# Kernel optimization log

Hardware: AMD Instinct MI355X
Metric: run time of the kernel (lower is better)

The kernel has to match this reference:

```python
import jax, jax.numpy as jnp
import numpy as np

B, L, D = 4, 4096, 1024  # batch, seq, d_model == in_features == out_features
E, R = 8, 8              # n_experts, r_base
DH = D // 2              # router hidden


def setup_inputs() -> dict:
    key = jax.random.key(0)
    ks = jax.random.split(key, 8)
    s = 0.02
    return {
        "x": jax.random.normal(ks[0], (B, L, D), dtype=jnp.float32),
        "W_base": jax.random.normal(ks[1], (D, D), dtype=jnp.float32) * s,
        "router_W1": jax.random.normal(ks[2], (DH, D), dtype=jnp.float32) * s,
        "router_b1": jnp.zeros((DH,), dtype=jnp.float32),
        "router_W2": jax.random.normal(ks[3], (E, DH), dtype=jnp.float32) * s,
        "router_b2": jnp.zeros((E,), dtype=jnp.float32),
        "temperature": jnp.asarray(1.0, dtype=jnp.float32),
        "lora_A": jax.random.normal(ks[4], (E, R, D), dtype=jnp.float32) * s,
        "lora_B": jax.random.normal(ks[5], (E, D, R), dtype=jnp.float32) * s,
    }


def reference(x, W_base, router_W1, router_b1, router_W2, router_b2,
              temperature, lora_A, lora_B):
    # Base frozen linear (bias=False): [B,L,D]
    base = jnp.einsum("bld,od->blo", x, W_base)
    # Router (eval mode: dropout inactive). hidden_states = x (Identity projection).
    h = jax.nn.relu(jnp.einsum("bld,hd->blh", x, router_W1) + router_b1)
    logits = (jnp.einsum("blh,eh->ble", h, router_W2) + router_b2) / temperature
    gates = jax.nn.softmax(logits, axis=-1)  # softmax over experts, [B,L,E]
    # All experts' low-rank projections batched: x @ A_e.T -> [B,L,E,R]
    xa = jnp.einsum("bld,erd->bler", x, lora_A)
    # Gate-weighted up-projection and sum over experts: [B,L,D]
    lora_out = jnp.einsum("bler,ble,edr->bld", xa, gates, lora_B)
    return base + lora_out
```

## Files before the change

kernel.cpp:

```cpp
#include <hip/hip_runtime.h>
#include <hip/hip_bf16.h>
#include <stdint.h>
#include <math.h>


#define M_TOK 16384

typedef unsigned short u16;
typedef short bf16x8 __attribute__((ext_vector_type(8)));
typedef float f32x4 __attribute__((ext_vector_type(4)));
typedef __attribute__((address_space(3))) uint32_t lds_u32_t;
typedef __attribute__((address_space(1))) const uint32_t glb_u32_t;

__device__ __forceinline__ u16 f2bf(float f) {
  uint32_t u = __builtin_bit_cast(uint32_t, f);
  return (u16)((u + 0x7fffu + ((u >> 16) & 1u)) >> 16);
}
__device__ __forceinline__ int cvtpk(float lo, float hi) {
  int r;
  asm("v_cvt_pk_bf16_f32 %0, %1, %2" : "=v"(r) : "v"(lo), "v"(hi));
  return r;
}

#define VMCNT(n) asm volatile("s_waitcnt vmcnt(%0)" ::"i"(n) : "memory")
#define LGKM0 asm volatile("s_waitcnt lgkmcnt(0)" ::: "memory")
#define BAR asm volatile("s_barrier" ::: "memory")
#define MEMFENCE asm volatile("" ::: "memory")
#define SP(x) __builtin_amdgcn_s_setprio(x)

__global__ __launch_bounds__(256) void prep_k(const float* __restrict__ Wb,
                                              const float* __restrict__ rW1,
                                              const float* __restrict__ rW2,
                                              const float* __restrict__ loraA,
                                              const float* __restrict__ loraB,
                                              u16* __restrict__ Btb,
                                              u16* __restrict__ W1b,
                                              u16* __restrict__ W2b,
                                              u16* __restrict__ A2b) {
  const int g = blockIdx.x;
  const int tid = threadIdx.x;
  if (g < 1024) {
    int i = g * 256 + tid;
    int idx = i * 4;
    int row = idx >> 10, col = idx & 1023;
    float4 v = ((const float4*)Wb)[i];
    ushort4 o;
    o.x = f2bf(v.x); o.y = f2bf(v.y); o.z = f2bf(v.z); o.w = f2bf(v.w);
    *(ushort4*)(Btb + (size_t)row * 1088 + col) = o;
  } else if (g < 1536) {
    int i = (g - 1024) * 256 + tid;
    float4 v = ((const float4*)rW1)[i];
    ushort4 o;
    o.x = f2bf(v.x); o.y = f2bf(v.y); o.z = f2bf(v.z); o.w = f2bf(v.w);
    ((ushort4*)W1b)[i] = o;
  } else if (g < 1792) {
    int idx = (g - 1536) * 256 + tid;
    int n = idx >> 6, q = idx & 63;
    int e = q >> 3, r = q & 7;
    Btb[(size_t)n * 1088 + 1024 + q] = f2bf(loraB[((size_t)(e * 1024 + n)) * 8 + r]);
  } else if (g < 1856) {
    int i = (g - 1792) * 256 + tid;
    float4 v = ((const float4*)loraA)[i];
    ushort4 o;
    o.x = f2bf(v.x); o.y = f2bf(v.y); o.z = f2bf(v.z); o.w = f2bf(v.w);
    ((ushort4*)A2b)[i] = o;
  } else {
    int i = (g - 1856) * 256 + tid;
    int idx = i * 4;
    int row = idx >> 9, col = idx & 511;
    ushort4 o = {0, 0, 0, 0};
    if (row < 8) {
      float4 v = *(const float4*)(rW2 + (size_t)row * 512 + col);
      o.x = f2bf(v.x); o.y = f2bf(v.y); o.z = f2bf(v.z); o.w = f2bf(v.w);
    }
    ((ushort4*)W2b)[i] = o;
  }
}

__global__ __launch_bounds__(512, 2) void gemm_h(const float* __restrict__ x,
                                                 const u16* __restrict__ W1b,
                                                 const u16* __restrict__ W2bv,
                                                 u16* __restrict__ xb,
                                                 float* __restrict__ gates,
                                                 const float* __restrict__ b1,
                                                 const float* __restrict__ b2,
                                                 const float* __restrict__ temp,
                                                 const int K) {
  constexpr int ABUF = 64 * 128;
  constexpr int BBUF = 512 * 128;
  constexpr int BUFB = ABUF + BBUF;
  __shared__ __align__(16) uint8_t lds[2 * BUFB];

  const int tid = threadIdx.x;
  const int lane = tid & 63, w = tid >> 6;
  const int l15 = lane & 15, lhi = lane >> 4;
  const int xorv = (lane & 7) << 4;
  const int c0 = (lhi * 16) ^ xorv;
  const int c1 = (64 + lhi * 16) ^ xorv;

  const int f = blockIdx.x;
  const int m0 = ((f & 7) * 32 + (f >> 3)) * 64;

  const int nk = K >> 6;
  const int rot = (f >> 3) & (nk - 1);
  auto PH = [&](int l) { int lc = l < nk ? l : nk - 1; return (lc + rot) & (nk - 1); };

  const int xrow = tid >> 3, xsub = tid & 7;

  f32x4 acc[4][4] = {};
  bf16x8 af[4][2], bfv[4][2];
  float4 xA0, xA1, xB0, xB1;

  auto stageBH = [&](int ktp, int b) {
    uint8_t* dst = lds + b * BUFB + ABUF + w * 1024;
#pragma unroll
    for (int i = 0; i < 8; ++i) {
      const int off = i * 8192 + tid * 16;
      const int row = off >> 7;
      const int ss = ((off >> 4) & 7) ^ (row & 7);
      const uint8_t* g =
          (const uint8_t*)W1b + (size_t)row * 2048 + ktp * 128 + ss * 16;
      __builtin_amdgcn_global_load_lds((glb_u32_t*)g, (lds_u32_t*)(dst + i * 8192),
                                       16, 0, 0);
    }
  };
  auto issueX = [&](int ktp, float4& ra, float4& rb) {
    const float* gp = x + (size_t)(m0 + xrow) * 1024 + ktp * 64 + xsub * 8;
    ra = *(const float4*)gp;
    rb = *(const float4*)(gp + 4);
  };
  auto writeA = [&](int ktp, int b, const float4& ra, const float4& rb) {
    int4 sv;
    sv.x = cvtpk(ra.x, ra.y); sv.y = cvtpk(ra.z, ra.w);
    sv.z = cvtpk(rb.x, rb.y); sv.w = cvtpk(rb.z, rb.w);
    *(int4*)(lds + b * BUFB + xrow * 128 + ((xsub ^ (xrow & 7)) << 4)) = sv;
    *(int4*)(xb + (size_t)(m0 + xrow) * 1024 + ktp * 64 + xsub * 8) = sv;
  };
  auto loadAH = [&](const uint8_t* bufA) {
#pragma unroll
    for (int mf = 0; mf < 4; ++mf) {
      const uint8_t* pr = bufA + (mf * 16 + l15) * 128;
      af[mf][0] = *(const bf16x8*)(pr + c0);
      af[mf][1] = *(const bf16x8*)(pr + c1);
    }
  };
  auto loadBH = [&](const uint8_t* bufB) {
#pragma unroll
    for (int nf = 0; nf < 4; ++nf) {
      const uint8_t* pr = bufB + (w * 64 + nf * 16 + l15) * 128;
      bfv[nf][0] = *(const bf16x8*)(pr + c0);
      bfv[nf][1] = *(const bf16x8*)(pr + c1);
    }
  };

#define HMM()                                                                  \
  _Pragma("unroll") for (int mf = 0; mf < 4; ++mf)                             \
  _Pragma("unroll") for (int nf = 0; nf < 4; ++nf)                             \
  _Pragma("unroll") for (int ks = 0; ks < 2; ++ks)                             \
      acc[mf][nf] = __builtin_amdgcn_mfma_f32_16x16x32_bf16(                   \
          af[mf][ks], bfv[nf][ks], acc[mf][nf], 0, 0, 0);

  {
    const float* gp = x + (size_t)(m0 + xrow) * 1024 + rot * 64 + xsub * 8;
    float4 a = *(const float4*)gp, b = *(const float4*)(gp + 4);
    int4 sv;
    sv.x = cvtpk(a.x, a.y); sv.y = cvtpk(a.z, a.w);
    sv.z = cvtpk(b.x, b.y); sv.w = cvtpk(b.z, b.w);
    *(int4*)(lds + xrow * 128 + ((xsub ^ (xrow & 7)) << 4)) = sv;
    *(int4*)(xb + (size_t)(m0 + xrow) * 1024 + rot * 64 + xsub * 8) = sv;
  }
  stageBH(rot, 0);
  MEMFENCE;
  issueX(PH(1), xA0, xA1);
  VMCNT(2);
  LGKM0;
  BAR;

  const int nit = nk >> 1;
#pragma unroll 1
  for (int it = 0; it < nit; ++it) {
    const int t = it * 2;
    loadAH(lds);
    loadBH(lds + ABUF);
    stageBH(PH(t + 1), 1);
    MEMFENCE;
    issueX(PH(t + 2), xB0, xB1);
    MEMFENCE;
    VMCNT(10);
    writeA(PH(t + 1), 1, xA0, xA1);
    SP(1); HMM(); SP(0);
    LGKM0; VMCNT(3); BAR;
    loadAH(lds + BUFB);
    loadBH(lds + BUFB + ABUF);
    stageBH(PH(t + 2), 0);
    MEMFENCE;
    issueX(PH(t + 3), xA0, xA1);
    MEMFENCE;
    VMCNT(10);
    writeA(PH(t + 2), 0, xB0, xB1);
    SP(1); HMM(); SP(0);
    LGKM0; VMCNT(3); BAR;
  }

  u16* hs = (u16*)lds;
  __syncthreads();
#pragma unroll
  for (int mf = 0; mf < 4; ++mf) {
#pragma unroll
    for (int nf = 0; nf < 4; ++nf) {
      const int col = w * 64 + nf * 16 + l15;
#pragma unroll
      for (int j = 0; j < 4; ++j) {
        const int row = mf * 16 + lhi * 4 + j;
        float v = fmaxf(acc[mf][nf][j] + b1[col], 0.f);
        hs[row * 520 + col] = f2bf(v);
      }
    }
  }
  __syncthreads();
  if (w < 4) {
    f32x4 acc2 = {};
#pragma unroll
    for (int ks = 0; ks < 16; ++ks) {
      bf16x8 bfrag = *(const bf16x8*)(W2bv + (size_t)l15 * 512 + ks * 32 + lhi * 8);
      bf16x8 afrag = *(const bf16x8*)(hs + (w * 16 + l15) * 520 + ks * 32 + lhi * 8);
      acc2 = __builtin_amdgcn_mfma_f32_16x16x32_bf16(afrag, bfrag, acc2, 0, 0, 0);
    }
    if (l15 < 8) {
      float t = temp[0];
      float lg[4];
#pragma unroll
      for (int j = 0; j < 4; ++j) lg[j] = (acc2[j] + b2[l15]) / t;
      float mx[4], sm[4];
#pragma unroll
      for (int j = 0; j < 4; ++j) mx[j] = lg[j];
#pragma unroll
      for (int m = 1; m <= 4; m <<= 1)
#pragma unroll
        for (int j = 0; j < 4; ++j) mx[j] = fmaxf(mx[j], __shfl_xor(mx[j], m));
#pragma unroll
      for (int j = 0; j < 4; ++j) { lg[j] = expf(lg[j] - mx[j]); sm[j] = lg[j]; }
#pragma unroll
      for (int m = 1; m <= 4; m <<= 1)
#pragma unroll
        for (int j = 0; j < 4; ++j) sm[j] += __shfl_xor(sm[j], m);
#pragma unroll
      for (int j = 0; j < 4; ++j)
        gates[(size_t)(m0 + w * 16 + lhi * 4 + j) * 8 + l15] = lg[j] / sm[j];
    }
  }
}

__global__ __launch_bounds__(256) void gemm_w(const u16* __restrict__ A,
                                              const u16* __restrict__ Bt,
                                              const float* __restrict__ gates,
                                              u16* __restrict__ Cv) {
  constexpr int BM = 64, BN = 64, FM = 2, FN = 2, AI = 2, BI = 2;
  __shared__ u16 lds[(BM + BN) * 64];
  __shared__ float g_lds[64][8];
  u16* As = lds;
  u16* Bs = lds + BM * 64;

  const int tid = threadIdx.x;
  const int w = tid >> 6, lane = tid & 63;
  const int wr = w >> 1, wc = w & 1;
  const int m0 = blockIdx.y * BM;

  if (tid < 64) {
    const float4* gp = (const float4*)(gates + (size_t)(m0 + tid) * 8);
    float4 a = gp[0], b = gp[1];
    g_lds[tid][0] = a.x; g_lds[tid][1] = a.y; g_lds[tid][2] = a.z; g_lds[tid][3] = a.w;
    g_lds[tid][4] = b.x; g_lds[tid][5] = b.y; g_lds[tid][6] = b.z; g_lds[tid][7] = b.w;
  }

  const uint8_t* Ab = (const uint8_t*)A;
  const uint8_t* Bb = (const uint8_t*)Bt;
  f32x4 acc[FM][FN] = {};

  for (int kt = 0; kt < 16; ++kt) {
#pragma unroll
    for (int i = 0; i < AI; ++i) {
      const int lbase = (w * AI + i) * 1024;
      const int o = lbase + lane * 16;
      const int r = o >> 7, cb = o & 127;
      const uint8_t* g = Ab + (size_t)(m0 + r) * 2048 + (size_t)kt * 128 + cb;
      __builtin_amdgcn_global_load_lds((glb_u32_t*)g,
                                       (lds_u32_t*)((uint8_t*)As + lbase), 16, 0, 0);
    }
#pragma unroll
    for (int i = 0; i < BI; ++i) {
      const int lbase = (w * BI + i) * 1024;
      const int o = lbase + lane * 16;
      const int r = o >> 7, cb = o & 127;
      const uint8_t* g = Bb + (size_t)r * 2048 + (size_t)kt * 128 + cb;
      __builtin_amdgcn_global_load_lds((glb_u32_t*)g,
                                       (lds_u32_t*)((uint8_t*)Bs + lbase), 16, 0, 0);
    }
    __syncthreads();

    bf16x8 af[2][FM], bfv[2][FN];
#pragma unroll
    for (int ks = 0; ks < 2; ++ks) {
      const int col = ks * 32 + ((lane >> 4) << 3);
#pragma unroll
      for (int im = 0; im < FM; ++im) {
        const int row = wr * 32 + im * 16 + (lane & 15);
        af[ks][im] = *(const bf16x8*)(As + row * 64 + col);
      }
#pragma unroll
      for (int in_ = 0; in_ < FN; ++in_) {
        const int row = wc * 32 + in_ * 16 + (lane & 15);
        bfv[ks][in_] = *(const bf16x8*)(Bs + row * 64 + col);
      }
    }
#pragma unroll
    for (int ks = 0; ks < 2; ++ks)
#pragma unroll
      for (int im = 0; im < FM; ++im)
#pragma unroll
        for (int in_ = 0; in_ < FN; ++in_)
          acc[im][in_] = __builtin_amdgcn_mfma_f32_16x16x32_bf16(
              af[ks][im], bfv[ks][in_], acc[im][in_], 0, 0, 0);
    __syncthreads();
  }

#pragma unroll
  for (int im = 0; im < FM; ++im)
#pragma unroll
    for (int in_ = 0; in_ < FN; ++in_) {
      const int col = wc * 32 + in_ * 16 + (lane & 15);
#pragma unroll
      for (int j = 0; j < 4; ++j) {
        const int lrow = wr * 32 + im * 16 + ((lane >> 4) << 2) + j;
        float v = acc[im][in_][j] * g_lds[lrow][col >> 3];
        Cv[(size_t)(m0 + lrow) * 64 + col] = f2bf(v);
      }
    }
}

#define MFMA_Q2(mh, nh, AF, BF)                                                \
  _Pragma("unroll") for (int im2 = 0; im2 < 4; ++im2)                          \
  _Pragma("unroll") for (int in2 = 0; in2 < 2; ++in2)                          \
  _Pragma("unroll") for (int ks = 0; ks < 2; ++ks)                             \
      acc[(mh) * 4 + im2][(nh) * 2 + in2] =                                    \
          __builtin_amdgcn_mfma_f32_16x16x32_bf16(                             \
              AF[im2][ks], BF[in2][ks],                                        \
              acc[(mh) * 4 + im2][(nh) * 2 + in2], 0, 0, 0);

__global__ __launch_bounds__(512, 2) void gemm_out(const u16* __restrict__ A,
                                                   const u16* __restrict__ Bt,
                                                   const u16* __restrict__ A2,
                                                   float* __restrict__ C,
                                                   const int N, const int K,
                                                   const int lda, const int ldb) {
  constexpr int BM = 256, BN = 256;
  constexpr int VMC = 4;
  constexpr int BUFB = (BM + BN) * 128;

  __shared__ __align__(16) uint8_t lds[2 * BUFB];

  const int tid = threadIdx.x;
  const int lane = tid & 63, w = tid >> 6;
  const int wr = w >> 2, wcn = w & 3;
  const int l15 = lane & 15, lhi = lane >> 4;
  const int xorv = (lane & 7) << 4;
  const int c0 = (lhi * 16) ^ xorv;
  const int c1 = (64 + lhi * 16) ^ xorv;

  const int f = blockIdx.x;
  const int idx = (f & 7) * 32 + (f >> 3);
  const int gx = N / BN;
  const int m0 = (idx / gx) * BM;
  const int n0 = (idx % gx) * BN;

  const size_t lda_b = (size_t)lda * 2, ldb_b = (size_t)ldb * 2;
  const int nk = K >> 6;
  const int arow0 = (wr * (BM / 2) + l15) * 128;
  const int brow0 = (wcn * (BN / 4) + l15) * 128;

  f32x4 acc[8][4] = {};
  bf16x8 A0f[4][2], A1f[4][2];
  bf16x8 B0f[2][2], B1f[2][2];

  auto stageA = [&](int h, int kt, int b) {
    const int ktc = kt < nk ? kt : nk - 1;
    const bool last = (ktc == nk - 1);
    uint8_t* dst = lds + b * BUFB + h * (BM * 64) + w * 1024;
#pragma unroll
    for (int i = 0; i < 2; ++i) {
      const int off = i * 8192 + tid * 16;
      const int row = h * (BM / 2) + (off >> 7);
      const int ss = ((off >> 4) & 7) ^ (row & 7);
      const uint8_t* g =
          last ? (const uint8_t*)A2 + (size_t)(m0 + row) * 128 + ss * 16
               : (const uint8_t*)A + (size_t)(m0 + row) * lda_b + ktc * 128 + ss * 16;
      __builtin_amdgcn_global_load_lds((glb_u32_t*)g, (lds_u32_t*)(dst + i * 8192),
                                       16, 0, 0);
    }
  };
  auto stageB = [&](int h, int kt, int b) {
    const int ktc = kt < nk ? kt : nk - 1;
    uint8_t* dst = lds + b * BUFB + BM * 128 + h * (BN * 64) + w * 1024;
#pragma unroll
    for (int i = 0; i < 2; ++i) {
      const int off = i * 8192 + tid * 16;
      const int row = h * (BN / 2) + (off >> 7);
      const int ss = ((off >> 4) & 7) ^ (row & 7);
      const uint8_t* g =
          (const uint8_t*)Bt + (size_t)(n0 + row) * ldb_b + ktc * 128 + ss * 16;
      __builtin_amdgcn_global_load_lds((glb_u32_t*)g, (lds_u32_t*)(dst + i * 8192),
                                       16, 0, 0);
    }
  };
  auto loadA = [&](int mh, const uint8_t* buf, bf16x8 (&dst)[4][2]) {
#pragma unroll
    for (int im2 = 0; im2 < 4; ++im2) {
      const uint8_t* p = buf + arow0 + mh * (4 * 2048) + im2 * 2048;
      dst[im2][0] = *(const bf16x8*)(p + c0);
      dst[im2][1] = *(const bf16x8*)(p + c1);
    }
  };
  auto loadB = [&](int nh, const uint8_t* buf, bf16x8 (&dst)[2][2]) {
#pragma unroll
    for (int in2 = 0; in2 < 2; ++in2) {
      const uint8_t* p = buf + BM * 128 + brow0 + nh * (2 * 2048) + in2 * 2048;
      dst[in2][0] = *(const bf16x8*)(p + c0);
      dst[in2][1] = *(const bf16x8*)(p + c1);
    }
  };

  const uint8_t* b0 = lds;
  const uint8_t* b1 = lds + BUFB;

  stageA(0, 0, 0); stageA(1, 0, 0);
  stageB(0, 0, 0); stageB(1, 0, 0);
  stageB(0, 1, 1); stageB(1, 1, 1);
  VMCNT(VMC); BAR;
  loadA(0, b0, A0f); loadB(0, b0, B0f);

  const int NIT = nk >> 1;
#pragma unroll 1
  for (int it = 0; it < NIT; ++it) {
    const int t = it * 2;
    stageA(0, t + 1, 1);
    BAR;
    SP(1); MFMA_Q2(0, 0, A0f, B0f); SP(0);
    loadB(1, b0, B1f);
    BAR;
    stageA(1, t + 1, 1);
    BAR;
    SP(1); MFMA_Q2(0, 1, A0f, B1f); SP(0);
    loadA(1, b0, A1f);
    BAR;
    stageB(0, t + 2, 0);
    BAR;
    SP(1); MFMA_Q2(1, 1, A1f, B1f); SP(0);
    BAR;
    stageB(1, t + 2, 0);
    VMCNT(VMC);
    BAR;
    SP(1); MFMA_Q2(1, 0, A1f, B0f); SP(0);
    loadA(0, b1, A0f); loadB(0, b1, B0f);
    BAR;
    stageA(0, t + 2, 0);
    BAR;
    SP(1); MFMA_Q2(0, 0, A0f, B0f); SP(0);
    loadB(1, b1, B1f);
    BAR;
    stageA(1, t + 2, 0);
    BAR;
    SP(1); MFMA_Q2(0, 1, A0f, B1f); SP(0);
    loadA(1, b1, A1f);
    BAR;
    stageB(0, t + 3, 1);
    BAR;
    SP(1); MFMA_Q2(1, 1, A1f, B1f); SP(0);
    BAR;
    stageB(1, t + 3, 1);
    VMCNT(VMC);
    BAR;
    SP(1); MFMA_Q2(1, 0, A1f, B0f); SP(0);
    loadA(0, b0, A0f); loadB(0, b0, B0f);
    BAR;
  }

  if (nk & 1) {
    SP(1); MFMA_Q2(0, 0, A0f, B0f); SP(0);
    loadB(1, b0, B1f);
    SP(1); MFMA_Q2(0, 1, A0f, B1f); SP(0);
    loadA(1, b0, A1f);
    SP(1); MFMA_Q2(1, 1, A1f, B1f); MFMA_Q2(1, 0, A1f, B0f); SP(0);
  }

#pragma unroll
  for (int im = 0; im < 8; ++im) {
#pragma unroll
    for (int in_ = 0; in_ < 4; ++in_) {
      const int col = n0 + wcn * 64 + in_ * 16 + l15;
#pragma unroll
      for (int j = 0; j < 4; ++j) {
        const int row = m0 + wr * 128 + im * 16 + lhi * 4 + j;
        C[(size_t)row * N + col] = acc[im][in_][j];
      }
    }
  }
}

extern "C" void kernel_launch(void* const* d_in, const int* in_sizes, int n_in,
                              void* d_out, int out_size, void* d_ws, size_t ws_size,
                              hipStream_t stream) {
  const float* x     = (const float*)d_in[0];
  const float* Wb    = (const float*)d_in[1];
  const float* rW1   = (const float*)d_in[2];
  const float* rb1   = (const float*)d_in[3];
  const float* rW2   = (const float*)d_in[4];
  const float* rb2   = (const float*)d_in[5];
  const float* temp  = (const float*)d_in[6];
  const float* loraA = (const float*)d_in[7];
  const float* loraB = (const float*)d_in[8];
  float* out = (float*)d_out;

  uint8_t* p = (uint8_t*)d_ws;
  u16* xb    = (u16*)p;   p += (size_t)M_TOK * 1024 * 2;
  u16* wb    = (u16*)p;   p += (size_t)M_TOK * 64 * 2;
  u16* Btb   = (u16*)p;   p += (size_t)1024 * 1088 * 2;
  u16* W1b   = (u16*)p;   p += (size_t)512 * 1024 * 2;
  u16* W2b   = (u16*)p;   p += (size_t)16 * 512 * 2;
  u16* A2b   = (u16*)p;   p += (size_t)64 * 1024 * 2;
  float* gates = (float*)p;

  prep_k<<<1864, 256, 0, stream>>>(Wb, rW1, rW2, loraA, loraB, Btb, W1b, W2b, A2b);

  gemm_h<<<256, 512, 0, stream>>>(x, W1b, W2b, xb, gates, rb1, rb2, temp, 1024);

  gemm_w<<<dim3(1, M_TOK / 64), 256, 0, stream>>>(xb, A2b, gates, wb);

  gemm_out<<<256, 512, 0, stream>>>(xb, Btb, wb, out, 1024, 1088, 1024, 1088);
}
```

Before: 90.33 us.

## Split router hidden GEMM over two N-halves and defer softmax to gemm_w

```diff
diff --git a/kernel.cpp b/kernel.cpp
--- a/kernel.cpp
+++ b/kernel.cpp
@@ -81,13 +81,11 @@
                                                  const u16* __restrict__ W1b,
                                                  const u16* __restrict__ W2bv,
                                                  u16* __restrict__ xb,
-                                                 float* __restrict__ gates,
+                                                 float* __restrict__ part,
                                                  const float* __restrict__ b1,
-                                                 const float* __restrict__ b2,
-                                                 const float* __restrict__ temp,
                                                  const int K) {
   constexpr int ABUF = 64 * 128;
-  constexpr int BBUF = 512 * 128;
+  constexpr int BBUF = 256 * 128;
   constexpr int BUFB = ABUF + BBUF;
   __shared__ __align__(16) uint8_t lds[2 * BUFB];
 
@@ -99,7 +97,9 @@
   const int c1 = (64 + lhi * 16) ^ xorv;
 
   const int f = blockIdx.x;
-  const int m0 = ((f & 7) * 32 + (f >> 3)) * 64;
+  const int idx = (f & 7) * 64 + (f >> 3);
+  const int m0 = (idx >> 1) * 64;
+  const int n0 = (idx & 1) * 256;
 
   const int nk = K >> 6;
   const int rot = (f >> 3) & (nk - 1);
@@ -107,19 +107,19 @@
 
   const int xrow = tid >> 3, xsub = tid & 7;
 
-  f32x4 acc[4][4] = {};
-  bf16x8 af[4][2], bfv[4][2];
+  f32x4 acc[4][2] = {};
+  bf16x8 af[4][2], bfv[2][2];
   float4 xA0, xA1, xB0, xB1;
 
   auto stageBH = [&](int ktp, int b) {
     uint8_t* dst = lds + b * BUFB + ABUF + w * 1024;
 #pragma unroll
-    for (int i = 0; i < 8; ++i) {
+    for (int i = 0; i < 4; ++i) {
       const int off = i * 8192 + tid * 16;
       const int row = off >> 7;
       const int ss = ((off >> 4) & 7) ^ (row & 7);
       const uint8_t* g =
-          (const uint8_t*)W1b + (size_t)row * 2048 + ktp * 128 + ss * 16;
+          (const uint8_t*)W1b + (size_t)(n0 + row) * 2048 + ktp * 128 + ss * 16;
       __builtin_amdgcn_global_load_lds((glb_u32_t*)g, (lds_u32_t*)(dst + i * 8192),
                                        16, 0, 0);
     }
@@ -146,8 +146,8 @@
   };
   auto loadBH = [&](const uint8_t* bufB) {
 #pragma unroll
-    for (int nf = 0; nf < 4; ++nf) {
-      const uint8_t* pr = bufB + (w * 64 + nf * 16 + l15) * 128;
+    for (int nf = 0; nf < 2; ++nf) {
+      const uint8_t* pr = bufB + (w * 32 + nf * 16 + l15) * 128;
       bfv[nf][0] = *(const bf16x8*)(pr + c0);
       bfv[nf][1] = *(const bf16x8*)(pr + c1);
     }
@@ -155,7 +155,7 @@
 
 #define HMM()                                                                  \
   _Pragma("unroll") for (int mf = 0; mf < 4; ++mf)                             \
-  _Pragma("unroll") for (int nf = 0; nf < 4; ++nf)                             \
+  _Pragma("unroll") for (int nf = 0; nf < 2; ++nf)                             \
   _Pragma("unroll") for (int ks = 0; ks < 2; ++ks)                             \
       acc[mf][nf] = __builtin_amdgcn_mfma_f32_16x16x32_bf16(                   \
           af[mf][ks], bfv[nf][ks], acc[mf][nf], 0, 0, 0);
@@ -186,7 +186,7 @@
     MEMFENCE;
     issueX(PH(t + 2), xB0, xB1);
     MEMFENCE;
-    VMCNT(10);
+    VMCNT(6);
     writeA(PH(t + 1), 1, xA0, xA1);
     SP(1); HMM(); SP(0);
     LGKM0; VMCNT(3); BAR;
@@ -196,7 +196,7 @@
     MEMFENCE;
     issueX(PH(t + 3), xA0, xA1);
     MEMFENCE;
-    VMCNT(10);
+    VMCNT(6);
     writeA(PH(t + 2), 0, xB0, xB1);
     SP(1); HMM(); SP(0);
     LGKM0; VMCNT(3); BAR;
@@ -207,13 +207,13 @@
 #pragma unroll
   for (int mf = 0; mf < 4; ++mf) {
 #pragma unroll
-    for (int nf = 0; nf < 4; ++nf) {
-      const int col = w * 64 + nf * 16 + l15;
+    for (int nf = 0; nf < 2; ++nf) {
+      const int col = w * 32 + nf * 16 + l15;
 #pragma unroll
       for (int j = 0; j < 4; ++j) {
         const int row = mf * 16 + lhi * 4 + j;
-        float v = fmaxf(acc[mf][nf][j] + b1[col], 0.f);
-        hs[row * 520 + col] = f2bf(v);
+        float v = fmaxf(acc[mf][nf][j] + b1[n0 + col], 0.f);
+        hs[row * 264 + col] = f2bf(v);
       }
     }
   }
@@ -221,39 +221,27 @@
   if (w < 4) {
     f32x4 acc2 = {};
 #pragma unroll
-    for (int ks = 0; ks < 16; ++ks) {
-      bf16x8 bfrag = *(const bf16x8*)(W2bv + (size_t)l15 * 512 + ks * 32 + lhi * 8);
-      bf16x8 afrag = *(const bf16x8*)(hs + (w * 16 + l15) * 520 + ks * 32 + lhi * 8);
+    for (int ks = 0; ks < 8; ++ks) {
+      bf16x8 bfrag = *(const bf16x8*)(W2bv + (size_t)l15 * 512 + n0 + ks * 32 + lhi * 8);
+      bf16x8 afrag = *(const bf16x8*)(hs + (w * 16 + l15) * 264 + ks * 32 + lhi * 8);
       acc2 = __builtin_amdgcn_mfma_f32_16x16x32_bf16(afrag, bfrag, acc2, 0, 0, 0);
     }
     if (l15 < 8) {
-      float t = temp[0];
-      float lg[4];
-#pragma unroll
-      for (int j = 0; j < 4; ++j) lg[j] = (acc2[j] + b2[l15]) / t;
-      float mx[4], sm[4];
-#pragma unroll
-      for (int j = 0; j < 4; ++j) mx[j] = lg[j];
-#pragma unroll
-      for (int m = 1; m <= 4; m <<= 1)
-#pragma unroll
-        for (int j = 0; j < 4; ++j) mx[j] = fmaxf(mx[j], __shfl_xor(mx[j], m));
-#pragma unroll
-      for (int j = 0; j < 4; ++j) { lg[j] = expf(lg[j] - mx[j]); sm[j] = lg[j]; }
-#pragma unroll
-      for (int m = 1; m <= 4; m <<= 1)
-#pragma unroll
-        for (int j = 0; j < 4; ++j) sm[j] += __shfl_xor(sm[j], m);
-#pragma unroll
-      for (int j = 0; j < 4; ++j)
-        gates[(size_t)(m0 + w * 16 + lhi * 4 + j) * 8 + l15] = lg[j] / sm[j];
+      const size_t base = (size_t)(n0 >> 8) * M_TOK;
+#pragma unroll
+      for (int j = 0; j < 4; ++j) {
+        const int row = m0 + w * 16 + lhi * 4 + j;
+        part[(base + row) * 8 + l15] = acc2[j];
+      }
     }
   }
 }
 
 __global__ __launch_bounds__(256) void gemm_w(const u16* __restrict__ A,
                                               const u16* __restrict__ Bt,
-                                              const float* __restrict__ gates,
+                                              const float* __restrict__ part,
+                                              const float* __restrict__ b2,
+                                              const float* __restrict__ temp,
                                               u16* __restrict__ Cv) {
   constexpr int BM = 64, BN = 64, FM = 2, FN = 2, AI = 2, BI = 2;
   __shared__ u16 lds[(BM + BN) * 64];
@@ -267,10 +255,24 @@
   const int m0 = blockIdx.y * BM;
 
   if (tid < 64) {
-    const float4* gp = (const float4*)(gates + (size_t)(m0 + tid) * 8);
-    float4 a = gp[0], b = gp[1];
-    g_lds[tid][0] = a.x; g_lds[tid][1] = a.y; g_lds[tid][2] = a.z; g_lds[tid][3] = a.w;
-    g_lds[tid][4] = b.x; g_lds[tid][5] = b.y; g_lds[tid][6] = b.z; g_lds[tid][7] = b.w;
+    const int m = m0 + tid;
+    float lg[8] = {};
+#pragma unroll
+    for (int q = 0; q < 2; ++q) {
+      const float4* pp = (const float4*)(part + ((size_t)q * M_TOK + m) * 8);
+      float4 a = pp[0], b = pp[1];
+      lg[0] += a.x; lg[1] += a.y; lg[2] += a.z; lg[3] += a.w;
+      lg[4] += b.x; lg[5] += b.y; lg[6] += b.z; lg[7] += b.w;
+    }
+    float t = temp[0], mx = -1e30f;
+#pragma unroll
+    for (int e = 0; e < 8; ++e) { lg[e] = (lg[e] + b2[e]) / t; mx = fmaxf(mx, lg[e]); }
+    float s = 0.f;
+#pragma unroll
+    for (int e = 0; e < 8; ++e) { lg[e] = expf(lg[e] - mx); s += lg[e]; }
+    float inv = 1.f / s;
+#pragma unroll
+    for (int e = 0; e < 8; ++e) g_lds[tid][e] = lg[e] * inv;
   }
 
   const uint8_t* Ab = (const uint8_t*)A;
@@ -527,13 +529,13 @@
   u16* W1b   = (u16*)p;   p += (size_t)512 * 1024 * 2;
   u16* W2b   = (u16*)p;   p += (size_t)16 * 512 * 2;
   u16* A2b   = (u16*)p;   p += (size_t)64 * 1024 * 2;
-  float* gates = (float*)p;
+  float* part = (float*)p;
 
   prep_k<<<1864, 256, 0, stream>>>(Wb, rW1, rW2, loraA, loraB, Btb, W1b, W2b, A2b);
 
-  gemm_h<<<256, 512, 0, stream>>>(x, W1b, W2b, xb, gates, rb1, rb2, temp, 1024);
-
-  gemm_w<<<dim3(1, M_TOK / 64), 256, 0, stream>>>(xb, A2b, gates, wb);
+  gemm_h<<<512, 512, 0, stream>>>(x, W1b, W2b, xb, part, rb1, 1024);
+
+  gemm_w<<<dim3(1, M_TOK / 64), 256, 0, stream>>>(xb, A2b, part, rb2, temp, wb);
 
   gemm_out<<<256, 512, 0, stream>>>(xb, Btb, wb, out, 1024, 1088, 1024, 1088);
 }
```

New measurement: 98.18 us. 8.7% more time.

## Fuse LoRA down-projection and gate scaling into router GEMM kernel

Applied to the files above, without the earlier changes.

```diff
diff --git a/kernel.cpp b/kernel.cpp
--- a/kernel.cpp
+++ b/kernel.cpp
@@ -80,15 +80,17 @@
 __global__ __launch_bounds__(512, 2) void gemm_h(const float* __restrict__ x,
                                                  const u16* __restrict__ W1b,
                                                  const u16* __restrict__ W2bv,
+                                                 const u16* __restrict__ A2bv,
                                                  u16* __restrict__ xb,
-                                                 float* __restrict__ gates,
+                                                 u16* __restrict__ wb,
                                                  const float* __restrict__ b1,
                                                  const float* __restrict__ b2,
                                                  const float* __restrict__ temp,
                                                  const int K) {
   constexpr int ABUF = 64 * 128;
   constexpr int BBUF = 512 * 128;
-  constexpr int BUFB = ABUF + BBUF;
+  constexpr int A2BUF = 64 * 128;
+  constexpr int BUFB = ABUF + BBUF + A2BUF;
   __shared__ __align__(16) uint8_t lds[2 * BUFB];
 
   const int tid = threadIdx.x;
@@ -108,7 +110,8 @@
   const int xrow = tid >> 3, xsub = tid & 7;
 
   f32x4 acc[4][4] = {};
-  bf16x8 af[4][2], bfv[4][2];
+  f32x4 wacc[4] = {};
+  bf16x8 af[4][2], bfv[4][2], a2f[2];
   float4 xA0, xA1, xB0, xB1;
 
   auto stageBH = [&](int ktp, int b) {
@@ -124,6 +127,15 @@
                                        16, 0, 0);
     }
   };
+  auto stageA2 = [&](int ktp, int b) {
+    uint8_t* dst = lds + b * BUFB + ABUF + BBUF + w * 1024;
+    const int off = tid * 16;
+    const int row = off >> 7;
+    const int ss = ((off >> 4) & 7) ^ (row & 7);
+    const uint8_t* g =
+        (const uint8_t*)A2bv + (size_t)row * 2048 + ktp * 128 + ss * 16;
+    __builtin_amdgcn_global_load_lds((glb_u32_t*)g, (lds_u32_t*)dst, 16, 0, 0);
+  };
   auto issueX = [&](int ktp, float4& ra, float4& rb) {
     const float* gp = x + (size_t)(m0 + xrow) * 1024 + ktp * 64 + xsub * 8;
     ra = *(const float4*)gp;
@@ -152,6 +164,11 @@
       bfv[nf][1] = *(const bf16x8*)(pr + c1);
     }
   };
+  auto loadA2 = [&](const uint8_t* base) {
+    const uint8_t* pr = base + ABUF + BBUF + ((w & 3) * 16 + l15) * 128;
+    a2f[0] = *(const bf16x8*)(pr + c0);
+    a2f[1] = *(const bf16x8*)(pr + c1);
+  };
 
 #define HMM()                                                                  \
   _Pragma("unroll") for (int mf = 0; mf < 4; ++mf)                             \
@@ -159,6 +176,11 @@
   _Pragma("unroll") for (int ks = 0; ks < 2; ++ks)                             \
       acc[mf][nf] = __builtin_amdgcn_mfma_f32_16x16x32_bf16(                   \
           af[mf][ks], bfv[nf][ks], acc[mf][nf], 0, 0, 0);
+#define WMM()                                                                  \
+  _Pragma("unroll") for (int mf = 0; mf < 4; ++mf)                             \
+  _Pragma("unroll") for (int ks = 0; ks < 2; ++ks)                             \
+      wacc[mf] = __builtin_amdgcn_mfma_f32_16x16x32_bf16(                      \
+          af[mf][ks], a2f[ks], wacc[mf], 0, 0, 0);
 
   {
     const float* gp = x + (size_t)(m0 + xrow) * 1024 + rot * 64 + xsub * 8;
@@ -170,6 +192,7 @@
     *(int4*)(xb + (size_t)(m0 + xrow) * 1024 + rot * 64 + xsub * 8) = sv;
   }
   stageBH(rot, 0);
+  stageA2(rot, 0);
   MEMFENCE;
   issueX(PH(1), xA0, xA1);
   VMCNT(2);
@@ -182,27 +205,32 @@
     const int t = it * 2;
     loadAH(lds);
     loadBH(lds + ABUF);
+    loadA2(lds);
     stageBH(PH(t + 1), 1);
+    stageA2(PH(t + 1), 1);
     MEMFENCE;
     issueX(PH(t + 2), xB0, xB1);
     MEMFENCE;
-    VMCNT(10);
+    VMCNT(11);
     writeA(PH(t + 1), 1, xA0, xA1);
-    SP(1); HMM(); SP(0);
+    SP(1); HMM(); WMM(); SP(0);
     LGKM0; VMCNT(3); BAR;
     loadAH(lds + BUFB);
     loadBH(lds + BUFB + ABUF);
+    loadA2(lds + BUFB);
     stageBH(PH(t + 2), 0);
+    stageA2(PH(t + 2), 0);
     MEMFENCE;
     issueX(PH(t + 3), xA0, xA1);
     MEMFENCE;
-    VMCNT(10);
+    VMCNT(11);
     writeA(PH(t + 2), 0, xB0, xB1);
-    SP(1); HMM(); SP(0);
+    SP(1); HMM(); WMM(); SP(0);
     LGKM0; VMCNT(3); BAR;
   }
 
   u16* hs = (u16*)lds;
+  float* g_lds = (float*)(lds + 66560);
   __syncthreads();
 #pragma unroll
   for (int mf = 0; mf < 4; ++mf) {
@@ -246,96 +274,22 @@
         for (int j = 0; j < 4; ++j) sm[j] += __shfl_xor(sm[j], m);
 #pragma unroll
       for (int j = 0; j < 4; ++j)
-        gates[(size_t)(m0 + w * 16 + lhi * 4 + j) * 8 + l15] = lg[j] / sm[j];
-    }
-  }
-}
-
-__global__ __launch_bounds__(256) void gemm_w(const u16* __restrict__ A,
-                                              const u16* __restrict__ Bt,
-                                              const float* __restrict__ gates,
-                                              u16* __restrict__ Cv) {
-  constexpr int BM = 64, BN = 64, FM = 2, FN = 2, AI = 2, BI = 2;
-  __shared__ u16 lds[(BM + BN) * 64];
-  __shared__ float g_lds[64][8];
-  u16* As = lds;
-  u16* Bs = lds + BM * 64;
-
-  const int tid = threadIdx.x;
-  const int w = tid >> 6, lane = tid & 63;
-  const int wr = w >> 1, wc = w & 1;
-  const int m0 = blockIdx.y * BM;
-
-  if (tid < 64) {
-    const float4* gp = (const float4*)(gates + (size_t)(m0 + tid) * 8);
-    float4 a = gp[0], b = gp[1];
-    g_lds[tid][0] = a.x; g_lds[tid][1] = a.y; g_lds[tid][2] = a.z; g_lds[tid][3] = a.w;
-    g_lds[tid][4] = b.x; g_lds[tid][5] = b.y; g_lds[tid][6] = b.z; g_lds[tid][7] = b.w;
-  }
-
-  const uint8_t* Ab = (const uint8_t*)A;
-  const uint8_t* Bb = (const uint8_t*)Bt;
-  f32x4 acc[FM][FN] = {};
-
-  for (int kt = 0; kt < 16; ++kt) {
-#pragma unroll
-    for (int i = 0; i < AI; ++i) {
-      const int lbase = (w * AI + i) * 1024;
-      const int o = lbase + lane * 16;
-      const int r = o >> 7, cb = o & 127;
-      const uint8_t* g = Ab + (size_t)(m0 + r) * 2048 + (size_t)kt * 128 + cb;
-      __builtin_amdgcn_global_load_lds((glb_u32_t*)g,
-                                       (lds_u32_t*)((uint8_t*)As + lbase), 16, 0, 0);
-    }
-#pragma unroll
-    for (int i = 0; i < BI; ++i) {
-      const int lbase = (w * BI + i) * 1024;
-      const int o = lbase + lane * 16;
-      const int r = o >> 7, cb = o & 127;
-      const uint8_t* g = Bb + (size_t)r * 2048 + (size_t)kt * 128 + cb;
-      __builtin_amdgcn_global_load_lds((glb_u32_t*)g,
-                                       (lds_u32_t*)((uint8_t*)Bs + lbase), 16, 0, 0);
-    }
-    __syncthreads();
-
-    bf16x8 af[2][FM], bfv[2][FN];
-#pragma unroll
-    for (int ks = 0; ks < 2; ++ks) {
-      const int col = ks * 32 + ((lane >> 4) << 3);
-#pragma unroll
-      for (int im = 0; im < FM; ++im) {
-        const int row = wr * 32 + im * 16 + (lane & 15);
-        af[ks][im] = *(const bf16x8*)(As + row * 64 + col);
+        g_lds[(w * 16 + lhi * 4 + j) * 8 + l15] = lg[j] / sm[j];
+    }
+  }
+  __syncthreads();
+  if (w < 4) {
+#pragma unroll
+    for (int mf = 0; mf < 4; ++mf) {
+#pragma unroll
+      for (int j = 0; j < 4; ++j) {
+        const int row = mf * 16 + lhi * 4 + j;
+        const int col = w * 16 + l15;
+        float v = wacc[mf][j] * g_lds[row * 8 + (col >> 3)];
+        wb[(size_t)(m0 + row) * 64 + col] = f2bf(v);
       }
-#pragma unroll
-      for (int in_ = 0; in_ < FN; ++in_) {
-        const int row = wc * 32 + in_ * 16 + (lane & 15);
-        bfv[ks][in_] = *(const bf16x8*)(Bs + row * 64 + col);
-      }
-    }
-#pragma unroll
-    for (int ks = 0; ks < 2; ++ks)
-#pragma unroll
-      for (int im = 0; im < FM; ++im)
-#pragma unroll
-        for (int in_ = 0; in_ < FN; ++in_)
-          acc[im][in_] = __builtin_amdgcn_mfma_f32_16x16x32_bf16(
-              af[ks][im], bfv[ks][in_], acc[im][in_], 0, 0, 0);
-    __syncthreads();
-  }
-
-#pragma unroll
-  for (int im = 0; im < FM; ++im)
-#pragma unroll
-    for (int in_ = 0; in_ < FN; ++in_) {
-      const int col = wc * 32 + in_ * 16 + (lane & 15);
-#pragma unroll
-      for (int j = 0; j < 4; ++j) {
-        const int lrow = wr * 32 + im * 16 + ((lane >> 4) << 2) + j;
-        float v = acc[im][in_][j] * g_lds[lrow][col >> 3];
-        Cv[(size_t)(m0 + lrow) * 64 + col] = f2bf(v);
-      }
-    }
+    }
+  }
 }
 
 #define MFMA_Q2(mh, nh, AF, BF)                                                \
@@ -527,13 +481,10 @@
   u16* W1b   = (u16*)p;   p += (size_t)512 * 1024 * 2;
   u16* W2b   = (u16*)p;   p += (size_t)16 * 512 * 2;
   u16* A2b   = (u16*)p;   p += (size_t)64 * 1024 * 2;
-  float* gates = (float*)p;
 
   prep_k<<<1864, 256, 0, stream>>>(Wb, rW1, rW2, loraA, loraB, Btb, W1b, W2b, A2b);
 
-  gemm_h<<<256, 512, 0, stream>>>(x, W1b, W2b, xb, gates, rb1, rb2, temp, 1024);
-
-  gemm_w<<<dim3(1, M_TOK / 64), 256, 0, stream>>>(xb, A2b, gates, wb);
+  gemm_h<<<256, 512, 0, stream>>>(x, W1b, W2b, A2b, xb, wb, rb1, rb2, temp, 1024);
 
   gemm_out<<<256, 512, 0, stream>>>(xb, Btb, wb, out, 1024, 1088, 1024, 1088);
 }
```

Result: faster. 81.54 us (-9.7%).
